# Kernel tuning notes

Measured on AMD Instinct MI355X. Metric: run time of the kernel, lower is better.

## Reference

```python
import jax, jax.numpy as jnp
import numpy as np

N_NODES = 4096
JACOBI_ITERS = 10
EPS = 1e-5


def sym_laplacian_dense(edge_index, n):
    # L = I - D^{-1/2} A D^{-1/2}, duplicates in edge_index accumulate (as scipy COO does)
    row, col = edge_index[0], edge_index[1]
    A = jnp.zeros((n, n), jnp.float32).at[row, col].add(1.0)
    deg = A.sum(axis=1)
    dinv = jnp.where(deg > 0, 1.0 / jnp.sqrt(jnp.where(deg > 0, deg, 1.0)), 0.0)
    return jnp.eye(n, dtype=jnp.float32) - dinv[:, None] * A * dinv[None, :]


def jacobi_eig(a, iterations):
    # Faithful Jacobi: `iterations` Givens rotations, each zeroing the max |off-diag| entry.
    n = a.shape[0]
    upper = jnp.triu(jnp.ones((n, n), bool), k=1)

    def body(_, carry):
        a, p = carry
        idx = jnp.argmax(jnp.where(upper, jnp.abs(a), 0.0))
        k, l = idx // n, idx % n
        akl = a[k, l]
        aDiff = a[l, l] - a[k, k]
        akl_safe = jnp.where(akl == 0.0, 1.0, akl)
        aDiff_safe = jnp.where(aDiff == 0.0, 1.0, aDiff)
        phi = aDiff / (2.0 * akl_safe)
        t2 = 1.0 / (jnp.abs(phi) + jnp.sqrt(phi * phi + 1.0))
        t2 = jnp.where(phi < 0.0, -t2, t2)
        t1 = akl / aDiff_safe
        t = jnp.where(jnp.abs(akl) < jnp.abs(aDiff) * 1e-36, t1, t2)
        c = 1.0 / jnp.sqrt(t * t + 1.0)
        s = t * c
        # a <- G^T a G  (equivalent to the triangular in-place updates for symmetric a)
        ck, cl = a[:, k], a[:, l]
        a = a.at[:, k].set(c * ck - s * cl).at[:, l].set(s * ck + c * cl)
        rk, rl = a[k, :], a[l, :]
        a = a.at[k, :].set(c * rk - s * rl).at[l, :].set(s * rk + c * rl)
        a = a.at[k, l].set(0.0).at[l, k].set(0.0)
        pk, pl = p[:, k], p[:, l]
        p = p.at[:, k].set(c * pk - s * pl).at[:, l].set(s * pk + c * pl)
        return a, p

    a, p = jax.lax.fori_loop(0, iterations, body, (a, jnp.eye(n, dtype=a.dtype)))
    return jnp.diagonal(a), p


def setup_inputs() -> dict:
    key = jax.random.key(0)
    ks = jax.random.split(key, 8)
    n, cin, cout, r, e = N_NODES, 64, 64, 4, 100000
    x = jax.random.normal(ks[0], (n, cin), jnp.float32)
    src = jax.random.randint(ks[1], (e,), 0, n)
    dst = jax.random.randint(ks[2], (e,), 0, n)
    # symmetric graph (undirected), as the Jacobi solver assumes a symmetric Laplacian
    edge_index = jnp.stack([jnp.concatenate([src, dst]), jnp.concatenate([dst, src])]).astype(jnp.int64)
    stdv = 1.0 / np.sqrt(cin)
    real_weight = jax.random.uniform(ks[3], (cout, cin, r, 1), jnp.float32, -stdv, stdv)
    imag_weight = jax.random.uniform(ks[4], (cout, cin, r, 1), jnp.float32, -stdv, stdv)
    h = jax.random.uniform(ks[5], (cout, cin), jnp.float32, -stdv, stdv)
    c = jax.random.uniform(ks[6], (cout, cin, 1), jnp.float32, -stdv, stdv)
    bias = jnp.zeros((cout,), jnp.float32)
    return {"x": x, "edge_index": edge_index, "real_weight": real_weight,
            "imag_weight": imag_weight, "h": h, "c": c, "bias": bias}


def reference(x, edge_index, real_weight, imag_weight, h, c, bias):
    n = x.shape[0]
    r = real_weight.shape[2]
    L = sym_laplacian_dense(edge_index, n)
    w, U = jacobi_eig(L, JACOBI_ITERS)          # w: (N,), U: (N, N)
    aux = U.T @ x                                # (N, in)
    hw = h[:, :, None] * w[None, None, :]        # (out, in, N)
    a2 = jnp.where(hw > EPS,
                   2.0 * jnp.arctan(1.0 / jnp.where(hw > EPS, hw, 1.0)),
                   2.0)
    # theta[o,i,j,n] = a2[o,i,n] * (j+1)  -> (out, in, r, N)
    theta = a2[:, :, None, :] * jnp.arange(1, r + 1, dtype=x.dtype)[None, None, :, None]
    g = real_weight * jnp.cos(theta) - imag_weight * jnp.sin(theta)
    g = g.sum(axis=2) + c                        # (out, in, N)
    out = jnp.einsum('oin,ni->on', g, aux)       # Pmul + sum over in-channels
    output = U @ out.T + bias                    # (N, out); note: original's clamp(min=0) is a no-op
    return output
```

## Files before the change

kernel.cpp:

```cpp
#include <hip/hip_runtime.h>
#include <hip/hip_bf16.h>

#pragma clang fp contract(off)

#define N 4096
#define CIN 64
#define COUT 64
#define ITERS 10
#define MAXS 40

typedef unsigned long long u64;

__device__ __forceinline__ u64 packkey(float v, unsigned j) {
    return ((u64)__float_as_uint(v) << 32) | (u64)(~j);
}

__global__ void init_k(int* __restrict__ deg, int* __restrict__ fill) {
    int i = blockIdx.x * 256 + threadIdx.x;
    if (i < N) { deg[i] = 0; fill[i] = 0; }
}

__global__ void edges1_k(const int* __restrict__ ei, int* __restrict__ deg, int E) {
    int e = blockIdx.x * 256 + threadIdx.x;
    if (e < E) atomicAdd(&deg[ei[e]], 1);
}

__global__ void __launch_bounds__(1024) scan_k(const int* __restrict__ deg,
                                               int* __restrict__ rowptr,
                                               float* __restrict__ dinv) {
    __shared__ int ps[1024];
    int t = threadIdx.x, b = t * 4;
    int d0 = deg[b], d1 = deg[b + 1], d2 = deg[b + 2], d3 = deg[b + 3];
    int local = d0 + d1 + d2 + d3;
    ps[t] = local;
    __syncthreads();
    for (int off = 1; off < 1024; off <<= 1) {
        int v = (t >= off) ? ps[t - off] : 0;
        __syncthreads();
        ps[t] += v;
        __syncthreads();
    }
    int excl = ps[t] - local;
    rowptr[b] = excl; rowptr[b + 1] = excl + d0;
    rowptr[b + 2] = excl + d0 + d1; rowptr[b + 3] = excl + d0 + d1 + d2;
    if (t == 1023) rowptr[4096] = ps[1023];
    dinv[b]     = d0 > 0 ? 1.0f / sqrtf((float)d0) : 0.0f;
    dinv[b + 1] = d1 > 0 ? 1.0f / sqrtf((float)d1) : 0.0f;
    dinv[b + 2] = d2 > 0 ? 1.0f / sqrtf((float)d2) : 0.0f;
    dinv[b + 3] = d3 > 0 ? 1.0f / sqrtf((float)d3) : 0.0f;
}

__global__ void edges2_k(const int* __restrict__ ei, const int* __restrict__ rowptr,
                         int* __restrict__ fill, int* __restrict__ colidx, int E) {
    int e = blockIdx.x * 256 + threadIdx.x;
    if (e < E) {
        int r = ei[e], c = ei[E + e];
        int pos = rowptr[r] + atomicAdd(&fill[r], 1);
        colidx[pos] = c;
    }
}

__global__ void prepw_k(const float* __restrict__ hh, const float* __restrict__ cw,
                        const float* __restrict__ rw, const float* __restrict__ iw,
                        float2* __restrict__ hcT, float4* __restrict__ rwT,
                        float4* __restrict__ iwT) {
    int idx = blockIdx.x * 256 + threadIdx.x;
    int i = idx >> 6, o = idx & 63;
    int src = o * 64 + i;
    hcT[idx] = make_float2(hh[src], cw[src]);
    rwT[idx] = make_float4(rw[src * 4 + 0], rw[src * 4 + 1], rw[src * 4 + 2], rw[src * 4 + 3]);
    iwT[idx] = make_float4(iw[src * 4 + 0], iw[src * 4 + 1], iw[src * 4 + 2], iw[src * 4 + 3]);
}

__global__ void __launch_bounds__(256) rowmax0_k(
        const int* __restrict__ rowptr, const int* __restrict__ colidx,
        const float* __restrict__ dinv, const float* __restrict__ x,
        float* __restrict__ y, float* __restrict__ diag,
        u64* __restrict__ rowmax, float* __restrict__ rowval) {
    const int i = blockIdx.x, t = threadIdx.x;
    __shared__ float row[N];
    __shared__ u64 w4[4];
    for (int j = i + t; j < N; j += 256) row[j] = 0.0f;
    __syncthreads();
    for (int e = rowptr[i] + t; e < rowptr[i + 1]; e += 256) {
        int c = colidx[e];
        if (c >= i) atomicAdd(&row[c], 1.0f);
    }
    __syncthreads();
    float di = dinv[i];
    u64 best = packkey(0.0f, 4095u);
    for (int j = i + 1 + t; j < N; j += 256) {
        float v = -((di * row[j]) * dinv[j]);
        u64 kk = packkey(fabsf(v), (unsigned)j);
        if (kk > best) best = kk;
    }
    for (int off = 32; off; off >>= 1) { u64 o = __shfl_down(best, off, 64); if (o > best) best = o; }
    if ((t & 63) == 0) w4[t >> 6] = best;
    __syncthreads();
    if (t == 0) {
        u64 b = w4[0];
        for (int w = 1; w < 4; ++w) if (w4[w] > b) b = w4[w];
        unsigned js = (~(unsigned)b) & 4095u;
        rowmax[i] = b;
        rowval[i] = -((di * row[js]) * dinv[js]);
        diag[i] = 1.0f - ((di * row[i]) * di);
    }
    if (t < CIN) y[i * CIN + t] = x[i * CIN + t];
}

__global__ void __launch_bounds__(1024) jacobi_k(
        const int* __restrict__ rowptr, const int* __restrict__ colidx,
        const float* __restrict__ dinv,
        float* __restrict__ diag, const u64* __restrict__ rowmaxG,
        const float* __restrict__ rowvalG, float* __restrict__ y,
        float* __restrict__ rowS, float* __restrict__ colS,
        int* __restrict__ dslotG, int* __restrict__ slistG, int* __restrict__ nslotsG,
        int* __restrict__ rotk, int* __restrict__ rotl,
        float* __restrict__ rotc, float* __restrict__ rotsv) {
    __shared__ float scratch4[4 * N];
    __shared__ u64 rmaxL[N];
    __shared__ float rvalL[N];
    __shared__ float diagL[N];
    __shared__ short dslotL[N];
    __shared__ unsigned short sdirty[N];
    __shared__ u64 w16[16], w16b[16];
    __shared__ float ovRowK[MAXS], ovRowL[MAXS], ovColK[MAXS], ovColL[MAXS];
    __shared__ float sgSub[4][2];
    __shared__ int slistL[MAXS];
    __shared__ int S_k, S_l, S_slotk, S_slotl, S_oldk, S_oldl, S_nold, S_ns, S_snd;
    __shared__ float S_c, S_s, S_a2kk, S_a2ll;
    const int t = threadIdx.x;
    float* cntK = scratch4;
    float* cntL = scratch4 + N;

    for (int i = t; i < N; i += 1024) {
        rmaxL[i] = rowmaxG[i];
        rvalL[i] = rowvalG[i];
        diagL[i] = diag[i];
        dslotL[i] = -1;
    }
    if (t == 0) S_ns = 0;
    __syncthreads();

    for (int it = 0; it < ITERS; ++it) {
        u64 best = 0ull;
        for (int r = t; r < N; r += 1024) {
            u64 p = rmaxL[r];
            unsigned vb = (unsigned)(p >> 32);
            unsigned j = (~(unsigned)p) & 4095u;
            unsigned flat = ((unsigned)r << 12) | j;
            u64 key = ((u64)vb << 24) | (u64)((~flat) & 0xFFFFFFu);
            if (key > best) best = key;
        }
        for (int off = 32; off; off >>= 1) { u64 o = __shfl_down(best, off, 64); if (o > best) best = o; }
        if ((t & 63) == 0) w16[t >> 6] = best;
        __syncthreads();
        if (t == 0) {
            u64 b = w16[0];
            for (int w = 1; w < 16; ++w) if (w16[w] > b) b = w16[w];
            unsigned flat = (~(unsigned)b) & 0xFFFFFFu;
            int k = (int)(flat >> 12), l = (int)(flat & 4095u);
            float akl = rvalL[k];
            float akk = diagL[k], all_ = diagL[l];
            float aDiff = all_ - akk;
            float akl_safe = (akl == 0.0f) ? 1.0f : akl;
            float aDiff_safe = (aDiff == 0.0f) ? 1.0f : aDiff;
            float phi = aDiff / (2.0f * akl_safe);
            float t2 = 1.0f / (fabsf(phi) + sqrtf(phi * phi + 1.0f));
            t2 = (phi < 0.0f) ? -t2 : t2;
            float t1 = akl / aDiff_safe;
            float tt = (fabsf(akl) < fabsf(aDiff) * 1e-36f) ? t1 : t2;
            float cv = 1.0f / sqrtf(tt * tt + 1.0f);
            float sv = tt * cv;
            rotk[it] = k; rotl[it] = l; rotc[it] = cv; rotsv[it] = sv;
            float a1kk = cv * akk - sv * akl;
            float a1kl = sv * akk + cv * akl;
            float a1lk = cv * akl - sv * all_;
            float a1ll = sv * akl + cv * all_;
            S_a2kk = cv * a1kk - sv * a1lk;
            S_a2ll = sv * a1kl + cv * a1ll;
            diagL[k] = S_a2kk; diagL[l] = S_a2ll;
            int ns = S_ns;
            S_nold = ns;
            int ok = dslotL[k]; S_oldk = ok;
            int sk = ok; if (ok < 0) { sk = ns; slistL[ns] = k; dslotL[k] = (short)ns; ns++; }
            int ol = dslotL[l]; S_oldl = ol;
            int sl = ol; if (ol < 0) { sl = ns; slistL[ns] = l; dslotL[l] = (short)ns; ns++; }
            S_ns = ns;
            S_k = k; S_l = l; S_slotk = sk; S_slotl = sl; S_c = cv; S_s = sv;
            S_snd = 0;
        }
        __syncthreads();
        const int k = S_k, l = S_l, slotk = S_slotk, slotl = S_slotl;
        const int oldk = S_oldk, oldl = S_oldl, nold = S_nold;
        const float c = S_c, s = S_s;
        const float a2kk = S_a2kk, a2ll = S_a2ll;
        const bool freshK = (oldk < 0), freshL = (oldl < 0);
        const float dk = dinv[k], dl = dinv[l];
        if (t < CIN) {
            float yk = y[k * CIN + t], yl = y[l * CIN + t];
            y[k * CIN + t] = c * yk - s * yl;
            y[l * CIN + t] = s * yk + c * yl;
        }
        if (t >= 64 && t < 64 + nold) {
            int sl2 = t - 64;
            if (freshK) { ovRowK[sl2] = colS[(size_t)sl2 * N + k]; ovColK[sl2] = rowS[(size_t)sl2 * N + k]; }
            if (freshL) { ovRowL[sl2] = colS[(size_t)sl2 * N + l]; ovColL[sl2] = rowS[(size_t)sl2 * N + l]; }
        }
        if (freshK) for (int j = t; j < N; j += 1024) cntK[j] = 0.0f;
        if (freshL) for (int j = t; j < N; j += 1024) cntL[j] = 0.0f;
        __syncthreads();
        if (freshK || freshL) {
            if (freshK) for (int e = rowptr[k] + t; e < rowptr[k + 1]; e += 1024) atomicAdd(&cntK[colidx[e]], 1.0f);
            if (freshL) for (int e = rowptr[l] + t; e < rowptr[l + 1]; e += 1024) atomicAdd(&cntL[colidx[e]], 1.0f);
            __syncthreads();
        }
        u64 bk = packkey(0.0f, 4095u), bl = packkey(0.0f, 4095u);
        {
            const int j0 = t * 4;
            float4 dj4 = *reinterpret_cast<const float4*>(dinv + j0);
            float4 bK4, bL4, cK4, cL4;
            if (freshK) {
                float4 cnt = *reinterpret_cast<const float4*>(cntK + j0);
#pragma unroll
                for (int m = 0; m < 4; ++m) {
                    float cn = (&cnt.x)[m], dj = (&dj4.x)[m];
                    (&bK4.x)[m] = -((dk * cn) * dj);
                    (&cK4.x)[m] = -((dj * cn) * dk);
                }
            } else {
                bK4 = *reinterpret_cast<const float4*>(rowS + (size_t)oldk * N + j0);
                cK4 = *reinterpret_cast<const float4*>(colS + (size_t)oldk * N + j0);
            }
            if (freshL) {
                float4 cnt = *reinterpret_cast<const float4*>(cntL + j0);
#pragma unroll
                for (int m = 0; m < 4; ++m) {
                    float cn = (&cnt.x)[m], dj = (&dj4.x)[m];
                    (&bL4.x)[m] = -((dl * cn) * dj);
                    (&cL4.x)[m] = -((dj * cn) * dl);
                }
            } else {
                bL4 = *reinterpret_cast<const float4*>(rowS + (size_t)oldl * N + j0);
                cL4 = *reinterpret_cast<const float4*>(colS + (size_t)oldl * N + j0);
            }
            float4 nrK4, nrL4, ncK4, ncL4;
#pragma unroll
            for (int m = 0; m < 4; ++m) {
                int j = j0 + m;
                float bK = (&bK4.x)[m], bL = (&bL4.x)[m];
                float cK = (&cK4.x)[m], cL = (&cL4.x)[m];
                float nrk, nrl, nck, ncl;
                if (j == k)      { nrk = a2kk; nrl = 0.0f; nck = a2kk; ncl = 0.0f; }
                else if (j == l) { nrk = 0.0f; nrl = a2ll; nck = 0.0f; ncl = a2ll; }
                else {
                    int sl2 = dslotL[j];
                    if (sl2 >= 0 && sl2 < nold) {
                        if (freshK) { bK = ovRowK[sl2]; cK = ovColK[sl2]; }
                        if (freshL) { bL = ovRowL[sl2]; cL = ovColL[sl2]; }
                    }
                    nrk = c * bK - s * bL; nrl = s * bK + c * bL;
                    nck = c * cK - s * cL; ncl = s * cK + c * cL;
                }
                (&nrK4.x)[m] = nrk; (&nrL4.x)[m] = nrl;
                (&ncK4.x)[m] = nck; (&ncL4.x)[m] = ncl;
                if (j > k) { u64 kk = packkey(fabsf(nrk), (unsigned)j); if (kk > bk) bk = kk; }
                if (j > l) { u64 kk = packkey(fabsf(nrl), (unsigned)j); if (kk > bl) bl = kk; }
                if (j != k && j != l) {
                    u64 cached = rmaxL[j];
                    unsigned cj = (~(unsigned)cached) & 4095u;
                    bool kc = (k > j), lc = (l > j);
                    u64 ckk = kc ? packkey(fabsf(nck), (unsigned)k) : 0ull;
                    u64 cll = lc ? packkey(fabsf(ncl), (unsigned)l) : 0ull;
                    bool stale = false; u64 base = cached; bool useOld = true;
                    if (kc && cj == (unsigned)k)      { if (ckk < cached) stale = true; else { base = 0ull; useOld = false; } }
                    else if (lc && cj == (unsigned)l) { if (cll < cached) stale = true; else { base = 0ull; useOld = false; } }
                    if (!stale) {
                        if (kc || lc) {
                            u64 mm = base; float mv = useOld ? rvalL[j] : 0.0f;
                            if (ckk > mm) { mm = ckk; mv = nck; }
                            if (cll > mm) { mm = cll; mv = ncl; }
                            rmaxL[j] = mm; rvalL[j] = mv;
                        }
                    } else {
                        int d = atomicAdd(&S_snd, 1);
                        sdirty[d] = (unsigned short)j;
                    }
                }
            }
            *reinterpret_cast<float4*>(rowS + (size_t)slotk * N + j0) = nrK4;
            *reinterpret_cast<float4*>(rowS + (size_t)slotl * N + j0) = nrL4;
            *reinterpret_cast<float4*>(colS + (size_t)slotk * N + j0) = ncK4;
            *reinterpret_cast<float4*>(colS + (size_t)slotl * N + j0) = ncL4;
        }
        for (int off = 32; off; off >>= 1) {
            u64 o = __shfl_down(bk, off, 64); if (o > bk) bk = o;
            u64 o2 = __shfl_down(bl, off, 64); if (o2 > bl) bl = o2;
        }
        if ((t & 63) == 0) { w16[t >> 6] = bk; w16b[t >> 6] = bl; }
        __syncthreads();
        if (t == 0) {
            u64 b1 = w16[0], b2 = w16b[0];
            for (int w = 1; w < 16; ++w) { if (w16[w] > b1) b1 = w16[w]; if (w16b[w] > b2) b2 = w16b[w]; }
            unsigned j1 = (~(unsigned)b1) & 4095u, j2 = (~(unsigned)b2) & 4095u;
            rmaxL[k] = b1; rvalL[k] = rowS[(size_t)slotk * N + j1];
            rmaxL[l] = b2; rvalL[l] = rowS[(size_t)slotl * N + j2];
        }
        if (t >= 64 && t < 64 + nold) {
            int sl2 = t - 64;
            int js = slistL[sl2];
            if (js != k && js != l) {
                colS[(size_t)sl2 * N + k] = rowS[(size_t)slotk * N + js];
                colS[(size_t)sl2 * N + l] = rowS[(size_t)slotl * N + js];
                rowS[(size_t)sl2 * N + k] = colS[(size_t)slotk * N + js];
                rowS[(size_t)sl2 * N + l] = colS[(size_t)slotl * N + js];
            }
        }
        __syncthreads();
        const int nd = S_snd;
        const int g = t >> 8, tl = t & 255;
        for (int r0 = 0; r0 < nd; r0 += 4) {
            int didx = r0 + g;
            int ir = -1, slot = -1;
            float di2 = 0.0f;
            bool active = (didx < nd);
            if (active) {
                ir = sdirty[didx];
                slot = dslotL[ir];
                di2 = dinv[ir];
            }
            float* sc = scratch4 + g * N;
            if (active && slot < 0) {
                for (int j = tl; j < N; j += 256) sc[j] = 0.0f;
            }
            if (active && tl == 0) {
                sgSub[g][0] = colS[(size_t)slotk * N + ir];
                sgSub[g][1] = colS[(size_t)slotl * N + ir];
            }
            __syncthreads();
            if (active && slot < 0) {
                for (int e = rowptr[ir] + tl; e < rowptr[ir + 1]; e += 256)
                    atomicAdd(&sc[colidx[e]], 1.0f);
            }
            __syncthreads();
            u64 bb = packkey(0.0f, 4095u);
            if (active) {
                float subK = sgSub[g][0], subL = sgSub[g][1];
                if (slot >= 0) {
                    for (int jb = tl * 4; jb < N; jb += 1024) {
                        float4 v4 = *reinterpret_cast<const float4*>(rowS + (size_t)slot * N + jb);
#pragma unroll
                        for (int m = 0; m < 4; ++m) {
                            int j = jb + m;
                            if (j <= ir) continue;
                            float v = (j == k) ? subK : (j == l) ? subL : (&v4.x)[m];
                            u64 kk = packkey(fabsf(v), (unsigned)j);
                            if (kk > bb) bb = kk;
                        }
                    }
                } else {
                    for (int jb = tl * 4; jb < N; jb += 1024) {
                        float4 c4 = *reinterpret_cast<const float4*>(sc + jb);
                        float4 d4 = *reinterpret_cast<const float4*>(dinv + jb);
#pragma unroll
                        for (int m = 0; m < 4; ++m) {
                            int j = jb + m;
                            if (j <= ir) continue;
                            int sl2 = dslotL[j];
                            float v = (sl2 >= 0) ? colS[(size_t)sl2 * N + ir]
                                                 : -((di2 * (&c4.x)[m]) * (&d4.x)[m]);
                            u64 kk = packkey(fabsf(v), (unsigned)j);
                            if (kk > bb) bb = kk;
                        }
                    }
                }
            }
            for (int off = 32; off; off >>= 1) { u64 o = __shfl_down(bb, off, 64); if (o > bb) bb = o; }
            if ((t & 63) == 0) w16[t >> 6] = bb;
            __syncthreads();
            if (active && tl == 0) {
                u64 b = w16[g * 4];
                for (int w = 1; w < 4; ++w) if (w16[g * 4 + w] > b) b = w16[g * 4 + w];
                unsigned js = (~(unsigned)b) & 4095u;
                rmaxL[ir] = b;
                float v;
                if (slot >= 0) {
                    v = (js == (unsigned)k) ? sgSub[g][0] : (js == (unsigned)l) ? sgSub[g][1]
                        : rowS[(size_t)slot * N + js];
                } else {
                    int sl2 = dslotL[js];
                    v = (sl2 >= 0) ? colS[(size_t)sl2 * N + ir]
                                   : -((di2 * sc[js]) * dinv[js]);
                }
                rvalL[ir] = v;
            }
            __syncthreads();
        }
    }
    for (int i = t; i < N; i += 1024) {
        diag[i] = diagL[i];
        dslotG[i] = (int)dslotL[i];
    }
    if (t < S_ns) slistG[t] = slistL[t];
    if (t == 0) *nslotsG = S_ns;
}

__global__ void __launch_bounds__(1024) spectral_k(
        const float* __restrict__ diag, const float* __restrict__ y,
        const float2* __restrict__ hcT, const float4* __restrict__ rwT,
        const float4* __restrict__ iwT, float* __restrict__ z) {
    int o = threadIdx.x & 63;
    int nl = threadIdx.x >> 6;
    int n = blockIdx.x * 16 + nl;
    __shared__ float saux[16][CIN];
    saux[nl][o] = y[n * CIN + o];
    __syncthreads();
    float wn = diag[n];
    const float C2 = -0.41614683654714241f;
    const float S2 = 0.90929742682568170f;
    float acc = 0.0f;
    for (int i = 0; i < CIN; ++i) {
        float2 hc = hcT[i * 64 + o];
        float hw = hc.x * wn;
        float t2v = hw * hw;
        float inv = 1.0f / (t2v + 1.0f);
        float c1 = (t2v - 1.0f) * inv;
        float s1 = (2.0f * hw) * inv;
        if (!(hw > 1e-5f)) { c1 = C2; s1 = S2; }
        float4 rwv = rwT[i * 64 + o];
        float4 iwv = iwT[i * 64 + o];
        float g = hc.y;
        float cj = c1, sj = s1;
        g += rwv.x * cj - iwv.x * sj;
        float cn = cj * c1 - sj * s1; float sn = sj * c1 + cj * s1; cj = cn; sj = sn;
        g += rwv.y * cj - iwv.y * sj;
        cn = cj * c1 - sj * s1; sn = sj * c1 + cj * s1; cj = cn; sj = sn;
        g += rwv.z * cj - iwv.z * sj;
        cn = cj * c1 - sj * s1; sn = sj * c1 + cj * s1; cj = cn; sj = sn;
        g += rwv.w * cj - iwv.w * sj;
        acc += g * saux[nl][i];
    }
    z[(size_t)n * COUT + o] = acc;
}

__global__ void store_fused_k(
        float* __restrict__ z, const float* __restrict__ bias,
        const int* __restrict__ dslot, const int* __restrict__ slistG,
        const int* __restrict__ nslotsG,
        const int* __restrict__ rotk, const int* __restrict__ rotl,
        const float* __restrict__ rotc, const float* __restrict__ rotsv,
        float* __restrict__ out) {
    int t = threadIdx.x;
    if (blockIdx.x < 1024) {
        int idx = blockIdx.x * 256 + t;
        int row = idx >> 6;
        if (dslot[row] < 0) out[idx] = z[idx] + bias[idx & 63];
    } else if (t < 64) {
        for (int i = ITERS - 1; i >= 0; --i) {
            int k = rotk[i], l = rotl[i];
            float c = rotc[i], s = rotsv[i];
            float zk = z[k * COUT + t];
            float zl = z[l * COUT + t];
            z[k * COUT + t] = c * zk + s * zl;
            z[l * COUT + t] = -s * zk + c * zl;
        }
        int ns = *nslotsG;
        for (int d = 0; d < ns; ++d) {
            int r = slistG[d];
            out[r * COUT + t] = z[r * COUT + t] + bias[t];
        }
    }
}

extern "C" void kernel_launch(void* const* d_in, const int* in_sizes, int n_in,
                              void* d_out, int out_size, void* d_ws, size_t ws_size,
                              hipStream_t stream) {
    const float* x   = (const float*)d_in[0];
    const int*   ei  = (const int*)d_in[1];
    const float* rw  = (const float*)d_in[2];
    const float* iw  = (const float*)d_in[3];
    const float* hh  = (const float*)d_in[4];
    const float* cw  = (const float*)d_in[5];
    const float* bias= (const float*)d_in[6];
    float* out = (float*)d_out;

    float* rowS = (float*)d_ws;
    float* colS = rowS + (size_t)MAXS * N;
    float* y    = colS + (size_t)MAXS * N;
    float* z    = y + N * CIN;
    float2* hcT = (float2*)(z + N * COUT);
    float4* rwT = (float4*)(hcT + 4096);
    float4* iwT = rwT + 4096;
    float* dinv = (float*)(iwT + 4096);
    float* diag = dinv + N;
    float* rowval = diag + N;
    u64* rowmax = (u64*)(rowval + N);
    int* rowptr = (int*)(rowmax + N);
    int* fill   = rowptr + 4100;
    int* deg    = fill + N;
    int* slist  = deg + N;
    int* nslots = slist + 64;
    int* dslot  = nslots + 4;
    int* rotk   = dslot + N;
    int* rotl   = rotk + 16;
    float* rotc = (float*)(rotl + 16);
    float* rotsv= rotc + 16;
    int* colidx = (int*)(rotsv + 16);

    int E = in_sizes[1] / 2;
    int eb = (E + 255) / 256;

    init_k<<<16, 256, 0, stream>>>(deg, fill);
    edges1_k<<<eb, 256, 0, stream>>>(ei, deg, E);
    scan_k<<<1, 1024, 0, stream>>>(deg, rowptr, dinv);
    edges2_k<<<eb, 256, 0, stream>>>(ei, rowptr, fill, colidx, E);
    prepw_k<<<16, 256, 0, stream>>>(hh, cw, rw, iw, hcT, rwT, iwT);
    rowmax0_k<<<N, 256, 0, stream>>>(rowptr, colidx, dinv, x, y, diag, rowmax, rowval);

    jacobi_k<<<1, 1024, 0, stream>>>(rowptr, colidx, dinv, diag, rowmax, rowval,
                                     y, rowS, colS, dslot, slist, nslots,
                                     rotk, rotl, rotc, rotsv);

    spectral_k<<<N / 16, 1024, 0, stream>>>(diag, y, hcT, rwT, iwT, z);
    store_fused_k<<<1025, 256, 0, stream>>>(z, bias, dslot, slist, nslots,
                                            rotk, rotl, rotc, rotsv, out);
}
```

Baseline: 284.6 us.

## Precompute per-row top-24 candidates and carry the pivot across Jacobi iterations

The per-row init kernel now touches only the nonzero columns and extracts a sorted top-24 candidate list per row, instead of scanning and clearing all 4096 columns. The Jacobi kernel computes the next pivot incrementally at the end of each iteration and keeps separate max keys for rows already touched by rotations. When an untouched row's cached max is invalidated, it is rebuilt from the stored candidates rather than from a shared-memory histogram of the sparse row. The weight-prep launch is also merged into the init kernel. This removes the dense per-row scans and the serial dirty-row rebuilds inside the single-block kernel. In exchange it adds 24 times N u64 of workspace and relies on 24 candidates per row staying sufficient.

```diff
diff --git a/kernel.cpp b/kernel.cpp
--- a/kernel.cpp
+++ b/kernel.cpp
@@ -7,17 +7,36 @@
 #define CIN 64
 #define COUT 64
 #define ITERS 10
-#define MAXS 40
+#define MAXS 32
+#define CANDMAX 384
 
 typedef unsigned long long u64;
 
 __device__ __forceinline__ u64 packkey(float v, unsigned j) {
     return ((u64)__float_as_uint(v) << 32) | (u64)(~j);
 }
-
-__global__ void init_k(int* __restrict__ deg, int* __restrict__ fill) {
-    int i = blockIdx.x * 256 + threadIdx.x;
-    if (i < N) { deg[i] = 0; fill[i] = 0; }
+__device__ __forceinline__ u64 gkey(unsigned vb, unsigned row, unsigned col) {
+    unsigned flat = (row << 12) | col;
+    return ((u64)vb << 24) | (u64)((~flat) & 0xFFFFFFu);
+}
+
+__global__ void init_prep_k(int* __restrict__ deg, int* __restrict__ fill,
+                            const float* __restrict__ hh, const float* __restrict__ cw,
+                            const float* __restrict__ rw, const float* __restrict__ iw,
+                            float2* __restrict__ hcT, float4* __restrict__ rwT,
+                            float4* __restrict__ iwT) {
+    int b = blockIdx.x;
+    if (b < 16) {
+        int i = b * 256 + threadIdx.x;
+        deg[i] = 0; fill[i] = 0;
+    } else {
+        int idx = (b - 16) * 256 + threadIdx.x;
+        int i = idx >> 6, o = idx & 63;
+        int src = o * 64 + i;
+        hcT[idx] = make_float2(hh[src], cw[src]);
+        rwT[idx] = make_float4(rw[src * 4 + 0], rw[src * 4 + 1], rw[src * 4 + 2], rw[src * 4 + 3]);
+        iwT[idx] = make_float4(iw[src * 4 + 0], iw[src * 4 + 1], iw[src * 4 + 2], iw[src * 4 + 3]);
+    }
 }
 
 __global__ void edges1_k(const int* __restrict__ ei, int* __restrict__ deg, int E) {
@@ -60,105 +79,88 @@
     }
 }
 
-__global__ void prepw_k(const float* __restrict__ hh, const float* __restrict__ cw,
-                        const float* __restrict__ rw, const float* __restrict__ iw,
-                        float2* __restrict__ hcT, float4* __restrict__ rwT,
-                        float4* __restrict__ iwT) {
-    int idx = blockIdx.x * 256 + threadIdx.x;
-    int i = idx >> 6, o = idx & 63;
-    int src = o * 64 + i;
-    hcT[idx] = make_float2(hh[src], cw[src]);
-    rwT[idx] = make_float4(rw[src * 4 + 0], rw[src * 4 + 1], rw[src * 4 + 2], rw[src * 4 + 3]);
-    iwT[idx] = make_float4(iw[src * 4 + 0], iw[src * 4 + 1], iw[src * 4 + 2], iw[src * 4 + 3]);
-}
-
-__global__ void __launch_bounds__(256) rowmax0_k(
+__global__ void __launch_bounds__(64) rowmax0_k(
         const int* __restrict__ rowptr, const int* __restrict__ colidx,
         const float* __restrict__ dinv, const float* __restrict__ x,
-        float* __restrict__ y, float* __restrict__ diag,
-        u64* __restrict__ rowmax, float* __restrict__ rowval) {
+        float* __restrict__ y, float* __restrict__ diag, u64* __restrict__ top24T) {
     const int i = blockIdx.x, t = threadIdx.x;
     __shared__ float row[N];
-    __shared__ u64 w4[4];
-    for (int j = i + t; j < N; j += 256) row[j] = 0.0f;
-    __syncthreads();
-    for (int e = rowptr[i] + t; e < rowptr[i + 1]; e += 256) {
-        int c = colidx[e];
-        if (c >= i) atomicAdd(&row[c], 1.0f);
-    }
+    __shared__ u64 cand[CANDMAX];
+    __shared__ int scnt;
+    int rs = rowptr[i], re = rowptr[i + 1];
+    if (t == 0) { scnt = 0; row[i] = 0.0f; }
+    __syncthreads();
+    for (int e = rs + t; e < re; e += 64) { int c2 = colidx[e]; if (c2 >= i) row[c2] = 0.0f; }
+    __syncthreads();
+    for (int e = rs + t; e < re; e += 64) { int c2 = colidx[e]; if (c2 >= i) atomicAdd(&row[c2], 1.0f); }
     __syncthreads();
     float di = dinv[i];
-    u64 best = packkey(0.0f, 4095u);
-    for (int j = i + 1 + t; j < N; j += 256) {
-        float v = -((di * row[j]) * dinv[j]);
-        u64 kk = packkey(fabsf(v), (unsigned)j);
-        if (kk > best) best = kk;
-    }
-    for (int off = 32; off; off >>= 1) { u64 o = __shfl_down(best, off, 64); if (o > best) best = o; }
-    if ((t & 63) == 0) w4[t >> 6] = best;
-    __syncthreads();
-    if (t == 0) {
-        u64 b = w4[0];
-        for (int w = 1; w < 4; ++w) if (w4[w] > b) b = w4[w];
-        unsigned js = (~(unsigned)b) & 4095u;
-        rowmax[i] = b;
-        rowval[i] = -((di * row[js]) * dinv[js]);
-        diag[i] = 1.0f - ((di * row[i]) * di);
-    }
-    if (t < CIN) y[i * CIN + t] = x[i * CIN + t];
+    for (int e = rs + t; e < re; e += 64) {
+        int c2 = colidx[e];
+        if (c2 > i) {
+            float v = -((di * row[c2]) * dinv[c2]);
+            int idx = atomicAdd(&scnt, 1);
+            if (idx < CANDMAX) cand[idx] = packkey(fabsf(v), (unsigned)c2);
+        }
+    }
+    __syncthreads();
+    int L = scnt < CANDMAX ? scnt : CANDMAX;
+    for (int r = 0; r < 24; ++r) {
+        u64 best = 0ull;
+        for (int idx = t; idx < L; idx += 64) { u64 cc = cand[idx]; if (cc > best) best = cc; }
+        for (int off = 32; off; off >>= 1) { u64 o = __shfl_xor(best, off, 64); if (o > best) best = o; }
+        if (t == 0) top24T[(size_t)r * N + i] = best;
+        for (int idx = t; idx < L; idx += 64) { if (cand[idx] == best) cand[idx] = 0ull; }
+        __syncthreads();
+    }
+    if (t == 0) diag[i] = 1.0f - ((di * row[i]) * di);
+    y[i * CIN + t] = x[i * CIN + t];
 }
 
 __global__ void __launch_bounds__(1024) jacobi_k(
         const int* __restrict__ rowptr, const int* __restrict__ colidx,
         const float* __restrict__ dinv,
-        float* __restrict__ diag, const u64* __restrict__ rowmaxG,
-        const float* __restrict__ rowvalG, float* __restrict__ y,
+        float* __restrict__ diag, const u64* __restrict__ top24T, float* __restrict__ y,
         float* __restrict__ rowS, float* __restrict__ colS,
         int* __restrict__ dslotG, int* __restrict__ slistG, int* __restrict__ nslotsG,
         int* __restrict__ rotk, int* __restrict__ rotl,
         float* __restrict__ rotc, float* __restrict__ rotsv) {
-    __shared__ float scratch4[4 * N];
+    __shared__ float cntK[N], cntL[N];
     __shared__ u64 rmaxL[N];
     __shared__ float rvalL[N];
     __shared__ float diagL[N];
     __shared__ short dslotL[N];
-    __shared__ unsigned short sdirty[N];
+    __shared__ u64 rmaxSlot[MAXS];
     __shared__ u64 w16[16], w16b[16];
     __shared__ float ovRowK[MAXS], ovRowL[MAXS], ovColK[MAXS], ovColL[MAXS];
-    __shared__ float sgSub[4][2];
     __shared__ int slistL[MAXS];
+    __shared__ unsigned short sdirty[64];
     __shared__ int S_k, S_l, S_slotk, S_slotl, S_oldk, S_oldl, S_nold, S_ns, S_snd;
     __shared__ float S_c, S_s, S_a2kk, S_a2ll;
+    __shared__ u64 S_pivot;
     const int t = threadIdx.x;
-    float* cntK = scratch4;
-    float* cntL = scratch4 + N;
-
+
+    u64 mb0 = 0ull;
     for (int i = t; i < N; i += 1024) {
-        rmaxL[i] = rowmaxG[i];
-        rvalL[i] = rowvalG[i];
+        u64 kk = top24T[i];
+        rmaxL[i] = kk;
+        rvalL[i] = -__uint_as_float((unsigned)(kk >> 32));
         diagL[i] = diag[i];
         dslotL[i] = -1;
+        unsigned col = (~(unsigned)kk) & 4095u;
+        u64 gk = gkey((unsigned)(kk >> 32), (unsigned)i, col);
+        if (gk > mb0) mb0 = gk;
     }
     if (t == 0) S_ns = 0;
+    for (int off = 32; off; off >>= 1) { u64 o = __shfl_down(mb0, off, 64); if (o > mb0) mb0 = o; }
+    if ((t & 63) == 0) w16[t >> 6] = mb0;
+    __syncthreads();
+    if (t == 0) { u64 b = w16[0]; for (int w = 1; w < 16; ++w) if (w16[w] > b) b = w16[w]; S_pivot = b; }
     __syncthreads();
 
     for (int it = 0; it < ITERS; ++it) {
-        u64 best = 0ull;
-        for (int r = t; r < N; r += 1024) {
-            u64 p = rmaxL[r];
-            unsigned vb = (unsigned)(p >> 32);
-            unsigned j = (~(unsigned)p) & 4095u;
-            unsigned flat = ((unsigned)r << 12) | j;
-            u64 key = ((u64)vb << 24) | (u64)((~flat) & 0xFFFFFFu);
-            if (key > best) best = key;
-        }
-        for (int off = 32; off; off >>= 1) { u64 o = __shfl_down(best, off, 64); if (o > best) best = o; }
-        if ((t & 63) == 0) w16[t >> 6] = best;
-        __syncthreads();
         if (t == 0) {
-            u64 b = w16[0];
-            for (int w = 1; w < 16; ++w) if (w16[w] > b) b = w16[w];
-            unsigned flat = (~(unsigned)b) & 0xFFFFFFu;
+            unsigned flat = (~(unsigned)S_pivot) & 0xFFFFFFu;
             int k = (int)(flat >> 12), l = (int)(flat & 4095u);
             float akl = rvalL[k];
             float akk = diagL[k], all_ = diagL[l];
@@ -183,16 +185,16 @@
             int ns = S_ns;
             S_nold = ns;
             int ok = dslotL[k]; S_oldk = ok;
-            int sk = ok; if (ok < 0) { sk = ns; slistL[ns] = k; dslotL[k] = (short)ns; ns++; }
+            int sk2 = ok; if (ok < 0) { sk2 = ns; slistL[ns] = k; dslotL[k] = (short)ns; ns++; }
             int ol = dslotL[l]; S_oldl = ol;
-            int sl = ol; if (ol < 0) { sl = ns; slistL[ns] = l; dslotL[l] = (short)ns; ns++; }
+            int sl3 = ol; if (ol < 0) { sl3 = ns; slistL[ns] = l; dslotL[l] = (short)ns; ns++; }
             S_ns = ns;
-            S_k = k; S_l = l; S_slotk = sk; S_slotl = sl; S_c = cv; S_s = sv;
+            S_k = k; S_l = l; S_slotk = sk2; S_slotl = sl3; S_c = cv; S_s = sv;
             S_snd = 0;
         }
         __syncthreads();
         const int k = S_k, l = S_l, slotk = S_slotk, slotl = S_slotl;
-        const int oldk = S_oldk, oldl = S_oldl, nold = S_nold;
+        const int oldk = S_oldk, oldl = S_oldl, nold = S_nold, ns = S_ns;
         const float c = S_c, s = S_s;
         const float a2kk = S_a2kk, a2ll = S_a2ll;
         const bool freshK = (oldk < 0), freshL = (oldl < 0);
@@ -266,32 +268,13 @@
                 (&ncK4.x)[m] = nck; (&ncL4.x)[m] = ncl;
                 if (j > k) { u64 kk = packkey(fabsf(nrk), (unsigned)j); if (kk > bk) bk = kk; }
                 if (j > l) { u64 kk = packkey(fabsf(nrl), (unsigned)j); if (kk > bl) bl = kk; }
-                if (j != k && j != l) {
-                    u64 cached = rmaxL[j];
-                    unsigned cj = (~(unsigned)cached) & 4095u;
-                    bool kc = (k > j), lc = (l > j);
-                    u64 ckk = kc ? packkey(fabsf(nck), (unsigned)k) : 0ull;
-                    u64 cll = lc ? packkey(fabsf(ncl), (unsigned)l) : 0ull;
-                    bool stale = false; u64 base = cached; bool useOld = true;
-                    if (kc && cj == (unsigned)k)      { if (ckk < cached) stale = true; else { base = 0ull; useOld = false; } }
-                    else if (lc && cj == (unsigned)l) { if (cll < cached) stale = true; else { base = 0ull; useOld = false; } }
-                    if (!stale) {
-                        if (kc || lc) {
-                            u64 mm = base; float mv = useOld ? rvalL[j] : 0.0f;
-                            if (ckk > mm) { mm = ckk; mv = nck; }
-                            if (cll > mm) { mm = cll; mv = ncl; }
-                            rmaxL[j] = mm; rvalL[j] = mv;
-                        }
-                    } else {
-                        int d = atomicAdd(&S_snd, 1);
-                        sdirty[d] = (unsigned short)j;
-                    }
-                }
             }
             *reinterpret_cast<float4*>(rowS + (size_t)slotk * N + j0) = nrK4;
             *reinterpret_cast<float4*>(rowS + (size_t)slotl * N + j0) = nrL4;
             *reinterpret_cast<float4*>(colS + (size_t)slotk * N + j0) = ncK4;
             *reinterpret_cast<float4*>(colS + (size_t)slotl * N + j0) = ncL4;
+            *reinterpret_cast<float4*>(cntK + j0) = ncK4;
+            *reinterpret_cast<float4*>(cntL + j0) = ncL4;
         }
         for (int off = 32; off; off >>= 1) {
             u64 o = __shfl_down(bk, off, 64); if (o > bk) bk = o;
@@ -303,99 +286,125 @@
             u64 b1 = w16[0], b2 = w16b[0];
             for (int w = 1; w < 16; ++w) { if (w16[w] > b1) b1 = w16[w]; if (w16b[w] > b2) b2 = w16b[w]; }
             unsigned j1 = (~(unsigned)b1) & 4095u, j2 = (~(unsigned)b2) & 4095u;
-            rmaxL[k] = b1; rvalL[k] = rowS[(size_t)slotk * N + j1];
-            rmaxL[l] = b2; rvalL[l] = rowS[(size_t)slotl * N + j2];
+            rvalL[k] = rowS[(size_t)slotk * N + j1];
+            rvalL[l] = rowS[(size_t)slotl * N + j2];
+            rmaxSlot[slotk] = gkey((unsigned)(b1 >> 32), (unsigned)k, j1);
+            rmaxSlot[slotl] = gkey((unsigned)(b2 >> 32), (unsigned)l, j2);
         }
         if (t >= 64 && t < 64 + nold) {
             int sl2 = t - 64;
             int js = slistL[sl2];
             if (js != k && js != l) {
-                colS[(size_t)sl2 * N + k] = rowS[(size_t)slotk * N + js];
-                colS[(size_t)sl2 * N + l] = rowS[(size_t)slotl * N + js];
-                rowS[(size_t)sl2 * N + k] = colS[(size_t)slotk * N + js];
-                rowS[(size_t)sl2 * N + l] = colS[(size_t)slotl * N + js];
-            }
+                float vkj = rowS[(size_t)slotk * N + js];
+                float vlj = rowS[(size_t)slotl * N + js];
+                float vjk = cntK[js];
+                float vjl = cntL[js];
+                colS[(size_t)sl2 * N + k] = vkj;
+                colS[(size_t)sl2 * N + l] = vlj;
+                rowS[(size_t)sl2 * N + k] = vjk;
+                rowS[(size_t)sl2 * N + l] = vjl;
+                u64 cached = rmaxSlot[sl2];
+                unsigned cj = ((~(unsigned)cached) & 0xFFFFFFu) & 4095u;
+                bool kc = (k > js), lc = (l > js);
+                u64 ck2 = kc ? gkey(__float_as_uint(fabsf(vjk)), (unsigned)js, (unsigned)k) : 0ull;
+                u64 cl2 = lc ? gkey(__float_as_uint(fabsf(vjl)), (unsigned)js, (unsigned)l) : 0ull;
+                bool stale = false; u64 base = cached; bool useOld = true;
+                if (kc && cj == (unsigned)k)      { if (ck2 < cached) stale = true; else { base = 0ull; useOld = false; } }
+                else if (lc && cj == (unsigned)l) { if (cl2 < cached) stale = true; else { base = 0ull; useOld = false; } }
+                if (!stale) {
+                    if (kc || lc) {
+                        u64 mm = base; float mv = useOld ? rvalL[js] : 0.0f;
+                        if (ck2 > mm) { mm = ck2; mv = vjk; }
+                        if (cl2 > mm) { mm = cl2; mv = vjl; }
+                        rmaxSlot[sl2] = mm; rvalL[js] = mv;
+                    }
+                } else { int d2 = atomicAdd(&S_snd, 1); sdirty[d2] = (unsigned short)sl2; }
+            }
+        }
+        u64 myBest = 0ull;
+#pragma unroll
+        for (int m = 0; m < 4; ++m) {
+            int j = t + 1024 * m;
+            if (j == k || j == l) continue;
+            if (dslotL[j] >= 0) continue;
+            float nck = cntK[j], ncl = cntL[j];
+            u64 cached = rmaxL[j];
+            unsigned cj = (~(unsigned)cached) & 4095u;
+            bool kc = (k > j), lc = (l > j);
+            u64 ck2 = kc ? packkey(fabsf(nck), (unsigned)k) : 0ull;
+            u64 cl2 = lc ? packkey(fabsf(ncl), (unsigned)l) : 0ull;
+            bool stale = false; u64 base = cached; bool useOld = true;
+            if (kc && cj == (unsigned)k)      { if (ck2 < cached) stale = true; else { base = 0ull; useOld = false; } }
+            else if (lc && cj == (unsigned)l) { if (cl2 < cached) stale = true; else { base = 0ull; useOld = false; } }
+            if (!stale) {
+                if (kc || lc) {
+                    u64 mm = base; float mv = useOld ? rvalL[j] : 0.0f;
+                    if (ck2 > mm) { mm = ck2; mv = nck; }
+                    if (cl2 > mm) { mm = cl2; mv = ncl; }
+                    rmaxL[j] = mm; rvalL[j] = mv;
+                }
+            } else {
+                u64 bKey = 0ull; float bVal = 0.0f;
+                for (int cc = 0; cc < 24; ++cc) {
+                    u64 cand = top24T[(size_t)cc * N + j];
+                    unsigned col = (~(unsigned)cand) & 4095u;
+                    if (dslotL[col] < 0) {
+                        bKey = cand;
+                        bVal = -__uint_as_float((unsigned)(cand >> 32));
+                        break;
+                    }
+                }
+                for (int sl = 0; sl < ns; ++sl) {
+                    if (sl == slotk || sl == slotl) continue;
+                    int js = slistL[sl];
+                    if (js > j) {
+                        float v = colS[(size_t)sl * N + j];
+                        u64 kk2 = packkey(fabsf(v), (unsigned)js);
+                        if (kk2 > bKey) { bKey = kk2; bVal = v; }
+                    }
+                }
+                if (kc && ck2 > bKey) { bKey = ck2; bVal = nck; }
+                if (lc && cl2 > bKey) { bKey = cl2; bVal = ncl; }
+                rmaxL[j] = bKey; rvalL[j] = bVal;
+            }
+            u64 fin = rmaxL[j];
+            u64 gk = gkey((unsigned)(fin >> 32), (unsigned)j, (~(unsigned)fin) & 4095u);
+            if (gk > myBest) myBest = gk;
         }
         __syncthreads();
         const int nd = S_snd;
-        const int g = t >> 8, tl = t & 255;
-        for (int r0 = 0; r0 < nd; r0 += 4) {
-            int didx = r0 + g;
-            int ir = -1, slot = -1;
-            float di2 = 0.0f;
-            bool active = (didx < nd);
-            if (active) {
-                ir = sdirty[didx];
-                slot = dslotL[ir];
-                di2 = dinv[ir];
-            }
-            float* sc = scratch4 + g * N;
-            if (active && slot < 0) {
-                for (int j = tl; j < N; j += 256) sc[j] = 0.0f;
-            }
-            if (active && tl == 0) {
-                sgSub[g][0] = colS[(size_t)slotk * N + ir];
-                sgSub[g][1] = colS[(size_t)slotl * N + ir];
-            }
-            __syncthreads();
-            if (active && slot < 0) {
-                for (int e = rowptr[ir] + tl; e < rowptr[ir + 1]; e += 256)
-                    atomicAdd(&sc[colidx[e]], 1.0f);
-            }
-            __syncthreads();
+        for (int d = 0; d < nd; ++d) {
+            int sl2 = sdirty[d];
+            int ir = slistL[sl2];
             u64 bb = packkey(0.0f, 4095u);
-            if (active) {
-                float subK = sgSub[g][0], subL = sgSub[g][1];
-                if (slot >= 0) {
-                    for (int jb = tl * 4; jb < N; jb += 1024) {
-                        float4 v4 = *reinterpret_cast<const float4*>(rowS + (size_t)slot * N + jb);
+            int jb = t * 4;
+            float4 v4 = *reinterpret_cast<const float4*>(rowS + (size_t)sl2 * N + jb);
 #pragma unroll
-                        for (int m = 0; m < 4; ++m) {
-                            int j = jb + m;
-                            if (j <= ir) continue;
-                            float v = (j == k) ? subK : (j == l) ? subL : (&v4.x)[m];
-                            u64 kk = packkey(fabsf(v), (unsigned)j);
-                            if (kk > bb) bb = kk;
-                        }
-                    }
-                } else {
-                    for (int jb = tl * 4; jb < N; jb += 1024) {
-                        float4 c4 = *reinterpret_cast<const float4*>(sc + jb);
-                        float4 d4 = *reinterpret_cast<const float4*>(dinv + jb);
-#pragma unroll
-                        for (int m = 0; m < 4; ++m) {
-                            int j = jb + m;
-                            if (j <= ir) continue;
-                            int sl2 = dslotL[j];
-                            float v = (sl2 >= 0) ? colS[(size_t)sl2 * N + ir]
-                                                 : -((di2 * (&c4.x)[m]) * (&d4.x)[m]);
-                            u64 kk = packkey(fabsf(v), (unsigned)j);
-                            if (kk > bb) bb = kk;
-                        }
-                    }
+            for (int m = 0; m < 4; ++m) {
+                int j = jb + m;
+                if (j > ir) {
+                    u64 kk = packkey(fabsf((&v4.x)[m]), (unsigned)j);
+                    if (kk > bb) bb = kk;
                 }
             }
             for (int off = 32; off; off >>= 1) { u64 o = __shfl_down(bb, off, 64); if (o > bb) bb = o; }
             if ((t & 63) == 0) w16[t >> 6] = bb;
             __syncthreads();
-            if (active && tl == 0) {
-                u64 b = w16[g * 4];
-                for (int w = 1; w < 4; ++w) if (w16[g * 4 + w] > b) b = w16[g * 4 + w];
-                unsigned js = (~(unsigned)b) & 4095u;
-                rmaxL[ir] = b;
-                float v;
-                if (slot >= 0) {
-                    v = (js == (unsigned)k) ? sgSub[g][0] : (js == (unsigned)l) ? sgSub[g][1]
-                        : rowS[(size_t)slot * N + js];
-                } else {
-                    int sl2 = dslotL[js];
-                    v = (sl2 >= 0) ? colS[(size_t)sl2 * N + ir]
-                                   : -((di2 * sc[js]) * dinv[js]);
-                }
-                rvalL[ir] = v;
+            if (t == 0) {
+                u64 b = w16[0];
+                for (int w = 1; w < 16; ++w) if (w16[w] > b) b = w16[w];
+                unsigned js2 = (~(unsigned)b) & 4095u;
+                rmaxSlot[sl2] = gkey((unsigned)(b >> 32), (unsigned)ir, js2);
+                rvalL[ir] = rowS[(size_t)sl2 * N + js2];
             }
             __syncthreads();
         }
+        if (t < ns) { u64 o = rmaxSlot[t]; if (o > myBest) myBest = o; }
+        for (int off = 32; off; off >>= 1) { u64 o = __shfl_down(myBest, off, 64); if (o > myBest) myBest = o; }
+        if ((t & 63) == 0) w16[t >> 6] = myBest;
+        __syncthreads();
+        if (t == 0) { u64 b = w16[0]; for (int w = 1; w < 16; ++w) if (w16[w] > b) b = w16[w]; S_pivot = b; }
+        __syncthreads();
     }
     for (int i = t; i < N; i += 1024) {
         diag[i] = diagL[i];
@@ -493,9 +502,8 @@
     float4* iwT = rwT + 4096;
     float* dinv = (float*)(iwT + 4096);
     float* diag = dinv + N;
-    float* rowval = diag + N;
-    u64* rowmax = (u64*)(rowval + N);
-    int* rowptr = (int*)(rowmax + N);
+    u64* top24T = (u64*)(diag + N);
+    int* rowptr = (int*)(top24T + 24 * (size_t)N);
     int* fill   = rowptr + 4100;
     int* deg    = fill + N;
     int* slist  = deg + N;
@@ -510,14 +518,13 @@
     int E = in_sizes[1] / 2;
     int eb = (E + 255) / 256;
 
-    init_k<<<16, 256, 0, stream>>>(deg, fill);
+    init_prep_k<<<32, 256, 0, stream>>>(deg, fill, hh, cw, rw, iw, hcT, rwT, iwT);
     edges1_k<<<eb, 256, 0, stream>>>(ei, deg, E);
     scan_k<<<1, 1024, 0, stream>>>(deg, rowptr, dinv);
     edges2_k<<<eb, 256, 0, stream>>>(ei, rowptr, fill, colidx, E);
-    prepw_k<<<16, 256, 0, stream>>>(hh, cw, rw, iw, hcT, rwT, iwT);
-    rowmax0_k<<<N, 256, 0, stream>>>(rowptr, colidx, dinv, x, y, diag, rowmax, rowval);
-
-    jacobi_k<<<1, 1024, 0, stream>>>(rowptr, colidx, dinv, diag, rowmax, rowval,
+    rowmax0_k<<<N, 64, 0, stream>>>(rowptr, colidx, dinv, x, y, diag, top24T);
+
+    jacobi_k<<<1, 1024, 0, stream>>>(rowptr, colidx, dinv, diag, top24T,
                                      y, rowS, colS, dslot, slist, nslots,
                                      rotk, rotl, rotc, rotsv);
 
```

New measurement: 264.1 us (median of 2 runs). 1.08x faster.
